# Optimization experiments

Measured on AMD Instinct MI355X. Metric: run time of the kernel, lower is better.

Reference implementation:

```python
import jax, jax.numpy as jnp
import numpy as np

N = 100000       # nodes
E = 1600000      # edges (avg degree 16)
F_IN = 128       # num_node_features
H = 128          # hidden_num
C = 40           # num_classes


def setup_inputs() -> dict:
    key = jax.random.key(0)
    k = jax.random.split(key, 6)
    x = jax.random.normal(k[0], (N, F_IN), dtype=jnp.float32)
    edge_index = jax.random.randint(k[1], (2, E), 0, N, dtype=jnp.int32)
    # Glorot-ish scaled params for the two GCNConv layers
    W1 = jax.random.normal(k[2], (F_IN, H), dtype=jnp.float32) * (1.0 / np.sqrt(F_IN))
    b1 = jnp.zeros((H,), dtype=jnp.float32)
    W2 = jax.random.normal(k[3], (H, C), dtype=jnp.float32) * (1.0 / np.sqrt(H))
    b2 = jnp.zeros((C,), dtype=jnp.float32)
    return {"x": x, "edge_index": edge_index, "W1": W1, "b1": b1, "W2": W2, "b2": b2}


def _gcn_conv(x, W, b, src, dst, n_nodes):
    """PyG GCNConv: add self-loops, symmetric normalization, linear transform.
    out[i] = sum_{j in N(i)} d_i^-1/2 d_j^-1/2 (x W)[j] + d_i^-1 (x W)[i] + b
    Self-loop contribution handled analytically (no edge concat).
    """
    h = x @ W                                            # [N, out]
    ones = jnp.ones((src.shape[0],), dtype=x.dtype)
    deg = jax.ops.segment_sum(ones, dst, num_segments=n_nodes) + 1.0  # +1 self-loop
    dinv = jax.lax.rsqrt(deg)                            # deg >= 1 always
    norm = dinv[src] * dinv[dst]                         # [E]
    msg = h[src] * norm[:, None]                         # [E, out] gather + scale
    agg = jax.ops.segment_sum(msg, dst, num_segments=n_nodes)
    agg = agg + h * (dinv * dinv)[:, None]               # self-loop term
    return agg + b


def reference(x, edge_index, W1, b1, W2, b2):
    # eval mode: F.dropout(training=False) is identity
    src, dst = edge_index[0], edge_index[1]
    h = jax.nn.relu(_gcn_conv(x, W1, b1, src, dst, N))
    out = _gcn_conv(h, W2, b2, src, dst, N)
    return out
```

## Files before the change

### kernel.cpp

```cpp
#include <hip/hip_runtime.h>
#include <hip/hip_fp16.h>


#define F_IN  128
#define F_H   128
#define F_OUT 40

#define BK_SHIFT 7
#define BK_MAX   1024
#define CHUNK    4096

typedef _Float16 half8v __attribute__((ext_vector_type(8)));
typedef float    f32x4  __attribute__((ext_vector_type(4)));


__global__ void k_prep(const float* __restrict__ W1, const float* __restrict__ W2,
                       __half* __restrict__ img1, __half* __restrict__ img2,
                       int* __restrict__ bcnt, int nbk) {
    int b = blockIdx.x;
    if (b < 64) {
        int idx = b * 256 + threadIdx.x;
        int j = idx >> 7, k = idx & 127;
        img1[j * 128 + (k ^ ((j & 7) << 3))] = __float2half_rn(W1[k * 128 + j]);
    } else if (b < 88) {
        int idx = (b - 64) * 256 + threadIdx.x;
        int j = idx >> 7, k = idx & 127;
        float v = (j < F_OUT) ? W2[k * F_OUT + j] : 0.f;
        img2[j * 128 + (k ^ ((j & 7) << 3))] = __float2half_rn(v);
    } else {
        for (int i = threadIdx.x; i < nbk; i += 256) bcnt[i] = 0;
    }
}


__global__ __launch_bounds__(256) void k_bscatter(const int* __restrict__ src,
                                                  const int* __restrict__ dst,
                                                  int* __restrict__ bcnt,
                                                  int* __restrict__ ebuf,
                                                  int e, int nbk, int cap) {
    __shared__ int hist[BK_MAX];
    __shared__ int base[BK_MAX];
    __shared__ int run[BK_MAX];
    int e0 = blockIdx.x * CHUNK;
    int e1 = min(e0 + CHUNK, e);
    for (int i = threadIdx.x; i < nbk; i += 256) { hist[i] = 0; run[i] = 0; }
    __syncthreads();
    for (int i = e0 + threadIdx.x; i < e1; i += 256)
        atomicAdd(&hist[dst[i] >> BK_SHIFT], 1);
    __syncthreads();
    for (int i = threadIdx.x; i < nbk; i += 256) {
        int c = hist[i];
        base[i] = c ? (cap * i + atomicAdd(&bcnt[i], c)) : 0;
    }
    __syncthreads();
    for (int i = e0 + threadIdx.x; i < e1; i += 256) {
        int d = dst[i];
        int b = d >> BK_SHIFT;
        int r = atomicAdd(&run[b], 1);
        ebuf[base[b] + r] = (src[i] << BK_SHIFT) | (d & ((1 << BK_SHIFT) - 1));
    }
}


__global__ __launch_bounds__(256) void k_bnode(const int* __restrict__ ebuf,
                                               const int* __restrict__ bcnt,
                                               int2* __restrict__ rbd,
                                               float* __restrict__ dinv,
                                               int* __restrict__ col,
                                               int n, int cap) {
    __shared__ int hist[128];
    __shared__ int sc[128];
    __shared__ int cur[128];
    const int b   = blockIdx.x;
    const int tid = threadIdx.x;
    const int e0 = b * cap;
    const int e1 = e0 + bcnt[b];

    if (tid < 128) hist[tid] = 0;
    __syncthreads();
    for (int i = e0 + tid; i < e1; i += 256)
        atomicAdd(&hist[ebuf[i] & 127], 1);
    __syncthreads();
    if (tid < 128) sc[tid] = hist[tid];
    __syncthreads();
    for (int off = 1; off < 128; off <<= 1) {
        int t = 0;
        if (tid < 128 && tid >= off) t = sc[tid - off];
        __syncthreads();
        if (tid < 128) sc[tid] += t;
        __syncthreads();
    }
    if (tid < 128) {
        int node = (b << BK_SHIFT) + tid;
        int excl = sc[tid] - hist[tid];
        if (node < n) {
            rbd[node] = make_int2(e0 + excl, hist[tid]);
            dinv[node] = rsqrtf((float)hist[tid] + 1.0f);
        }
        cur[tid] = e0 + excl;
    }
    __syncthreads();
    for (int i = e0 + tid; i < e1; i += 256) {
        int w = ebuf[i];
        int pos = atomicAdd(&cur[w & 127], 1);
        col[pos] = w >> BK_SHIFT;
    }
}


__global__ __launch_bounds__(256) void k_gemm1(const float* __restrict__ x,
                                               const __half* __restrict__ Wimg,
                                               const float* __restrict__ dinv,
                                               __half* __restrict__ h, int n) {
    __shared__ __half wlds[128 * 128];
    const int tid = threadIdx.x;
#pragma unroll
    for (int it = 0; it < 8; ++it) {
        int i = tid * 8 + it * 2048;
        *(uint4*)&wlds[i] = *(const uint4*)&Wimg[i];
    }

    const int l  = tid & 63;
    const int g  = l >> 4;
    const int r0 = blockIdx.x * 64 + (tid >> 6) * 16;
    int row = r0 + (l & 15);
    if (row > n - 1) row = n - 1;

    const float* xb = x + row * F_IN + g * 8;
    half8v afr[4];
#pragma unroll
    for (int kk = 0; kk < 4; ++kk) {
        float4 u0 = *(const float4*)(xb + kk * 32);
        float4 u1 = *(const float4*)(xb + kk * 32 + 4);
        half8v a;
        a[0] = (_Float16)u0.x; a[1] = (_Float16)u0.y;
        a[2] = (_Float16)u0.z; a[3] = (_Float16)u0.w;
        a[4] = (_Float16)u1.x; a[5] = (_Float16)u1.y;
        a[6] = (_Float16)u1.z; a[7] = (_Float16)u1.w;
        afr[kk] = a;
    }
    __syncthreads();

    const char* wb = (const char*)wlds;
    const int swz = (l & 7) << 4;
    f32x4 acc[8] = {};
#pragma unroll
    for (int ct = 0; ct < 8; ++ct) {
        const int base = (ct * 16 + (l & 15)) * 256;
#pragma unroll
        for (int kk = 0; kk < 4; ++kk) {
            half8v bfr = *(const half8v*)(wb + base + ((kk * 64 + g * 16) ^ swz));
            acc[ct] = __builtin_amdgcn_mfma_f32_16x16x32_f16(afr[kk], bfr, acc[ct], 0, 0, 0);
        }
    }

    const int orow0 = r0 + g * 4;
    float dv[4];
#pragma unroll
    for (int b = 0; b < 4; ++b) {
        int r = orow0 + b;
        dv[b] = (r < n) ? dinv[r] : 0.f;
    }
#pragma unroll
    for (int ct = 0; ct < 8; ++ct) {
#pragma unroll
        for (int b = 0; b < 4; ++b) {
            int r = orow0 + b;
            if (r < n)
                h[r * F_H + ct * 16 + (l & 15)] = __float2half_rn(acc[ct][b] * dv[b]);
        }
    }
}


#define UNPK8(A, u) { \
    float2 t0 = __half22float2(*(__half2*)&(u).x); \
    float2 t1 = __half22float2(*(__half2*)&(u).y); \
    float2 t2 = __half22float2(*(__half2*)&(u).z); \
    float2 t3 = __half22float2(*(__half2*)&(u).w); \
    A[0] += t0.x; A[1] += t0.y; A[2] += t1.x; A[3] += t1.y; \
    A[4] += t2.x; A[5] += t2.y; A[6] += t3.x; A[7] += t3.y; }

__global__ __launch_bounds__(256) void k_agg1r(const __half* __restrict__ h1s,
                                               const int2* __restrict__ rbd,
                                               const int* __restrict__ col,
                                               const float* __restrict__ dinv,
                                               const float* __restrict__ b1,
                                               __half* __restrict__ out1, int n) {
    int wid = (blockIdx.x * 256 + threadIdx.x) >> 6;
    int lane = threadIdx.x & 63;
    if (wid >= n) return;
    int2 bd = rbd[wid];
    int beg = bd.x, end = bd.x + bd.y;
    const int q = lane >> 4;
    const int f = lane & 15;
    const uint4* hb = (const uint4*)h1s + f;

    float ax[8] = {}, bx[8] = {};
    int idx = beg;
    for (; idx + 8 <= end; idx += 8) {
        int s0 = col[idx + q];
        int s1 = col[idx + 4 + q];
        uint4 u0 = hb[s0 << 4];
        uint4 u1 = hb[s1 << 4];
        UNPK8(ax, u0);
        UNPK8(bx, u1);
    }
    if (idx + 4 <= end) {
        int s = col[idx + q];
        uint4 u = hb[s << 4];
        UNPK8(ax, u);
        idx += 4;
    }
    int rem = end - idx;
    if (q < rem) {
        int s = col[idx + q];
        uint4 u = hb[s << 4];
        UNPK8(bx, u);
    }
#pragma unroll
    for (int j = 0; j < 8; ++j) ax[j] += bx[j];
#pragma unroll
    for (int j = 0; j < 8; ++j) {
        ax[j] += __shfl(ax[j], lane ^ 16);
        ax[j] += __shfl(ax[j], lane ^ 32);
    }
    if (q == 0) {
        uint4 hu = hb[wid << 4];
        float hv[8] = {};
        UNPK8(hv, hu);
        float di = dinv[wid];
        float4 bv0 = *(const float4*)&b1[8 * f];
        float4 bv1 = *(const float4*)&b1[8 * f + 4];
        float o[8];
        o[0] = fmaxf(fmaf(ax[0] + hv[0], di, bv0.x), 0.f);
        o[1] = fmaxf(fmaf(ax[1] + hv[1], di, bv0.y), 0.f);
        o[2] = fmaxf(fmaf(ax[2] + hv[2], di, bv0.z), 0.f);
        o[3] = fmaxf(fmaf(ax[3] + hv[3], di, bv0.w), 0.f);
        o[4] = fmaxf(fmaf(ax[4] + hv[4], di, bv1.x), 0.f);
        o[5] = fmaxf(fmaf(ax[5] + hv[5], di, bv1.y), 0.f);
        o[6] = fmaxf(fmaf(ax[6] + hv[6], di, bv1.z), 0.f);
        o[7] = fmaxf(fmaf(ax[7] + hv[7], di, bv1.w), 0.f);
        __half2 p0 = __floats2half2_rn(o[0], o[1]);
        __half2 p1 = __floats2half2_rn(o[2], o[3]);
        __half2 p2 = __floats2half2_rn(o[4], o[5]);
        __half2 p3 = __floats2half2_rn(o[6], o[7]);
        uint4 pk;
        pk.x = *(unsigned int*)&p0; pk.y = *(unsigned int*)&p1;
        pk.z = *(unsigned int*)&p2; pk.w = *(unsigned int*)&p3;
        *(uint4*)&out1[(wid << 7) + 8 * f] = pk;
    }
}


__global__ __launch_bounds__(256) void k_gemm2(const __half* __restrict__ xin,
                                               const __half* __restrict__ Wimg,
                                               const float* __restrict__ dinv,
                                               __half* __restrict__ h, int n) {
    __shared__ __half wlds[48 * 128];
    const int tid = threadIdx.x;
#pragma unroll
    for (int it = 0; it < 3; ++it) {
        int i = tid * 8 + it * 2048;
        *(uint4*)&wlds[i] = *(const uint4*)&Wimg[i];
    }

    const int l  = tid & 63;
    const int g  = l >> 4;
    const int r0 = blockIdx.x * 64 + (tid >> 6) * 16;
    int row = r0 + (l & 15);
    if (row > n - 1) row = n - 1;

    const __half* ab = xin + row * F_H + g * 8;
    half8v afr[4];
#pragma unroll
    for (int kk = 0; kk < 4; ++kk) afr[kk] = *(const half8v*)(ab + kk * 32);
    __syncthreads();

    const char* wb = (const char*)wlds;
    const int swz = (l & 7) << 4;
    f32x4 acc[3] = {};
#pragma unroll
    for (int ct = 0; ct < 3; ++ct) {
        const int base = (ct * 16 + (l & 15)) * 256;
#pragma unroll
        for (int kk = 0; kk < 4; ++kk) {
            half8v bfr = *(const half8v*)(wb + base + ((kk * 64 + g * 16) ^ swz));
            acc[ct] = __builtin_amdgcn_mfma_f32_16x16x32_f16(afr[kk], bfr, acc[ct], 0, 0, 0);
        }
    }

    const int orow0 = r0 + g * 4;
    float dv[4];
#pragma unroll
    for (int b = 0; b < 4; ++b) {
        int r = orow0 + b;
        dv[b] = (r < n) ? dinv[r] : 0.f;
    }
#pragma unroll
    for (int ct = 0; ct < 3; ++ct) {
        int c = ct * 16 + (l & 15);
#pragma unroll
        for (int b = 0; b < 4; ++b) {
            int r = orow0 + b;
            if (r < n && c < F_OUT)
                h[r * F_OUT + c] = __float2half_rn(acc[ct][b] * dv[b]);
        }
    }
}


#define UNPK4(A, u) { \
    float2 t0 = __half22float2(*(__half2*)&(u).x); \
    float2 t1 = __half22float2(*(__half2*)&(u).y); \
    A[0] += t0.x; A[1] += t0.y; A[2] += t1.x; A[3] += t1.y; }

__global__ __launch_bounds__(256) void k_agg2(const __half* __restrict__ h2s,
                                              const int2* __restrict__ rbd,
                                              const int* __restrict__ col,
                                              const float* __restrict__ dinv,
                                              const float* __restrict__ b2,
                                              float* __restrict__ out, int n) {
    int wid = (blockIdx.x * 256 + threadIdx.x) >> 6;
    int lane = threadIdx.x & 63;
    if (wid >= n) return;
    int g = lane / 10;
    int f = lane - g * 10;
    bool act = (g < 6);
    const uint2* hb = (const uint2*)h2s + f;
    int2 bd = rbd[wid];
    int beg = bd.x, end = bd.x + bd.y;

    float ax[4] = {}, bx[4] = {};
    int idx = beg;
    if (act) {
        for (; idx + 12 <= end; idx += 12) {
            int s0 = col[idx + g];
            int s1 = col[idx + 6 + g];
            uint2 u0 = hb[s0 * 10];
            uint2 u1 = hb[s1 * 10];
            UNPK4(ax, u0);
            UNPK4(bx, u1);
        }
        if (idx + 6 <= end) {
            int s = col[idx + g];
            uint2 u = hb[s * 10];
            UNPK4(ax, u);
            idx += 6;
        }
        int rem = end - idx;
        if (g < rem) {
            int s = col[idx + g];
            uint2 u = hb[s * 10];
            UNPK4(bx, u);
        }
    }
#pragma unroll
    for (int j = 0; j < 4; ++j) ax[j] += bx[j];
#pragma unroll
    for (int j = 0; j < 4; ++j) {
        float t = ax[j] + __shfl(ax[j], lane + 30);
        ax[j] = t + __shfl(t, lane + 10) + __shfl(t, lane + 20);
    }
    if (g == 0) {
        uint2 hu = hb[wid * 10];
        float hv[4] = {};
        UNPK4(hv, hu);
        float di = dinv[wid];
        float4 bv = *(const float4*)&b2[4 * f];
        float4 o;
        o.x = fmaf(ax[0] + hv[0], di, bv.x);
        o.y = fmaf(ax[1] + hv[1], di, bv.y);
        o.z = fmaf(ax[2] + hv[2], di, bv.z);
        o.w = fmaf(ax[3] + hv[3], di, bv.w);
        *(float4*)&out[wid * F_OUT + 4 * f] = o;
    }
}


extern "C" void kernel_launch(void* const* d_in, const int* in_sizes, int n_in,
                              void* d_out, int out_size, void* d_ws, size_t ws_size,
                              hipStream_t stream) {
    const float* x  = (const float*)d_in[0];
    const int*   ei = (const int*)d_in[1];
    const float* W1 = (const float*)d_in[2];
    const float* b1 = (const float*)d_in[3];
    const float* W2 = (const float*)d_in[4];
    const float* b2 = (const float*)d_in[5];
    float* out = (float*)d_out;

    const int N = in_sizes[0] / F_IN;
    const int E = in_sizes[1] / 2;
    const int* src = ei;
    const int* dst = ei + E;
    const int nbk = (N + (1 << BK_SHIFT) - 1) >> BK_SHIFT;
    const int cap = (((2 * E) / nbk) + 63) & ~63;

    char* ws = (char*)d_ws;
    size_t off = 0;
    auto alloc = [&](size_t bytes) -> void* {
        off = (off + 255) & ~(size_t)255;
        void* p = ws + off;
        off += bytes;
        return p;
    };
    float*  dinv    = (float*) alloc((size_t)N * 4);
    int2*   rbd     = (int2*)  alloc((size_t)N * 8);
    int*    bcnt    = (int*)   alloc(BK_MAX * 4);
    __half* W1img   = (__half*)alloc(128 * 128 * 2);
    __half* W2img   = (__half*)alloc(48 * 128 * 2);
    int*    ebuf    = (int*)   alloc((size_t)nbk * cap * 4);
    int*    col     = (int*)   alloc((size_t)nbk * cap * 4);
    __half* h1s     = (__half*)alloc((size_t)N * F_H * 2);
    __half* out1h   = (__half*)alloc((size_t)N * F_H * 2);
    __half* h2s     = h1s;

    const int gC = (E + CHUNK - 1) / CHUNK;

    k_prep    <<<89, 256, 0, stream>>>(W1, W2, W1img, W2img, bcnt, nbk);
    k_bscatter<<<gC, 256, 0, stream>>>(src, dst, bcnt, ebuf, E, nbk, cap);
    k_bnode   <<<nbk, 256, 0, stream>>>(ebuf, bcnt, rbd, dinv, col, N, cap);

    k_gemm1<<<(N + 63) / 64, 256, 0, stream>>>(x, W1img, dinv, h1s, N);
    k_agg1r<<<(N + 3) / 4, 256, 0, stream>>>(h1s, rbd, col, dinv, b1, out1h, N);
    k_gemm2<<<(N + 63) / 64, 256, 0, stream>>>(out1h, W2img, dinv, h2s, N);
    k_agg2 <<<(N + 3) / 4, 256, 0, stream>>>(h2s, rbd, col, dinv, b2, out, N);
}
```

Before: 185.2 us.

## Slice layer-1 features into 16-column blocks for cache-friendly aggregation

Stores the first GEMM output in a column-sliced layout: eight slices of 16 halves per node. Aggregation becomes a persistent-grid kernel where blockIdx selects a slice, so each slice's gathers work over a 3.2MB table that fits better in cache. The second GEMM reads its A operand from the same sliced layout. The cost is 8-byte gathers instead of 16-byte ones, each node's col list being read eight times, and more shuffle reductions.

```diff
diff --git a/kernel.cpp b/kernel.cpp
--- a/kernel.cpp
+++ b/kernel.cpp
@@ -167,88 +167,72 @@
         for (int b = 0; b < 4; ++b) {
             int r = orow0 + b;
             if (r < n)
-                h[r * F_H + ct * 16 + (l & 15)] = __float2half_rn(acc[ct][b] * dv[b]);
-        }
-    }
-}
-
-
-#define UNPK8(A, u) { \
-    float2 t0 = __half22float2(*(__half2*)&(u).x); \
-    float2 t1 = __half22float2(*(__half2*)&(u).y); \
-    float2 t2 = __half22float2(*(__half2*)&(u).z); \
-    float2 t3 = __half22float2(*(__half2*)&(u).w); \
-    A[0] += t0.x; A[1] += t0.y; A[2] += t1.x; A[3] += t1.y; \
-    A[4] += t2.x; A[5] += t2.y; A[6] += t3.x; A[7] += t3.y; }
-
-__global__ __launch_bounds__(256) void k_agg1r(const __half* __restrict__ h1s,
+                h[(size_t)ct * n * 16 + r * 16 + (l & 15)] =
+                    __float2half_rn(acc[ct][b] * dv[b]);
+        }
+    }
+}
+
+
+__global__ __launch_bounds__(256) void k_agg1s(const __half* __restrict__ hs,
                                                const int2* __restrict__ rbd,
                                                const int* __restrict__ col,
                                                const float* __restrict__ dinv,
                                                const float* __restrict__ b1,
-                                               __half* __restrict__ out1, int n) {
-    int wid = (blockIdx.x * 256 + threadIdx.x) >> 6;
-    int lane = threadIdx.x & 63;
-    if (wid >= n) return;
-    int2 bd = rbd[wid];
-    int beg = bd.x, end = bd.x + bd.y;
-    const int q = lane >> 4;
-    const int f = lane & 15;
-    const uint4* hb = (const uint4*)h1s + f;
-
-    float ax[8] = {}, bx[8] = {};
-    int idx = beg;
-    for (; idx + 8 <= end; idx += 8) {
-        int s0 = col[idx + q];
-        int s1 = col[idx + 4 + q];
-        uint4 u0 = hb[s0 << 4];
-        uint4 u1 = hb[s1 << 4];
-        UNPK8(ax, u0);
-        UNPK8(bx, u1);
-    }
-    if (idx + 4 <= end) {
-        int s = col[idx + q];
-        uint4 u = hb[s << 4];
-        UNPK8(ax, u);
-        idx += 4;
-    }
-    int rem = end - idx;
-    if (q < rem) {
-        int s = col[idx + q];
-        uint4 u = hb[s << 4];
-        UNPK8(bx, u);
-    }
-#pragma unroll
-    for (int j = 0; j < 8; ++j) ax[j] += bx[j];
-#pragma unroll
-    for (int j = 0; j < 8; ++j) {
-        ax[j] += __shfl(ax[j], lane ^ 16);
-        ax[j] += __shfl(ax[j], lane ^ 32);
-    }
-    if (q == 0) {
-        uint4 hu = hb[wid << 4];
-        float hv[8] = {};
-        UNPK8(hv, hu);
-        float di = dinv[wid];
-        float4 bv0 = *(const float4*)&b1[8 * f];
-        float4 bv1 = *(const float4*)&b1[8 * f + 4];
-        float o[8];
-        o[0] = fmaxf(fmaf(ax[0] + hv[0], di, bv0.x), 0.f);
-        o[1] = fmaxf(fmaf(ax[1] + hv[1], di, bv0.y), 0.f);
-        o[2] = fmaxf(fmaf(ax[2] + hv[2], di, bv0.z), 0.f);
-        o[3] = fmaxf(fmaf(ax[3] + hv[3], di, bv0.w), 0.f);
-        o[4] = fmaxf(fmaf(ax[4] + hv[4], di, bv1.x), 0.f);
-        o[5] = fmaxf(fmaf(ax[5] + hv[5], di, bv1.y), 0.f);
-        o[6] = fmaxf(fmaf(ax[6] + hv[6], di, bv1.z), 0.f);
-        o[7] = fmaxf(fmaf(ax[7] + hv[7], di, bv1.w), 0.f);
-        __half2 p0 = __floats2half2_rn(o[0], o[1]);
-        __half2 p1 = __floats2half2_rn(o[2], o[3]);
-        __half2 p2 = __floats2half2_rn(o[4], o[5]);
-        __half2 p3 = __floats2half2_rn(o[6], o[7]);
-        uint4 pk;
-        pk.x = *(unsigned int*)&p0; pk.y = *(unsigned int*)&p1;
-        pk.z = *(unsigned int*)&p2; pk.w = *(unsigned int*)&p3;
-        *(uint4*)&out1[(wid << 7) + 8 * f] = pk;
+                                               __half* __restrict__ outs,
+                                               int n, int nslcblk) {
+    const int slice = blockIdx.x & 7;
+    const int blk   = blockIdx.x >> 3;
+    const int wave  = threadIdx.x >> 6;
+    const int lane  = threadIdx.x & 63;
+    const int q = lane >> 2;
+    const int p = lane & 3;
+
+    const uint2* t = (const uint2*)hs + (size_t)slice * n * 4 + p;
+    __half* os = outs + (size_t)slice * n * 16;
+    const int wps = nslcblk * 4;
+
+    for (int node = blk * 4 + wave; node < n; node += wps) {
+        int2 bd = rbd[node];
+        int beg = bd.x, end = beg + bd.y;
+
+        float a0 = 0.f, a1 = 0.f, a2 = 0.f, a3 = 0.f;
+        for (int idx = beg; idx < end; idx += 16) {
+            int sl = idx + q;
+            if (sl < end) {
+                int s = col[sl];
+                uint2 u = t[s << 2];
+                float2 u0 = __half22float2(*(__half2*)&u.x);
+                float2 u1 = __half22float2(*(__half2*)&u.y);
+                a0 += u0.x; a1 += u0.y; a2 += u1.x; a3 += u1.y;
+            }
+        }
+        a0 += __shfl(a0, lane ^ 4);  a1 += __shfl(a1, lane ^ 4);
+        a2 += __shfl(a2, lane ^ 4);  a3 += __shfl(a3, lane ^ 4);
+        a0 += __shfl(a0, lane ^ 8);  a1 += __shfl(a1, lane ^ 8);
+        a2 += __shfl(a2, lane ^ 8);  a3 += __shfl(a3, lane ^ 8);
+        a0 += __shfl(a0, lane ^ 16); a1 += __shfl(a1, lane ^ 16);
+        a2 += __shfl(a2, lane ^ 16); a3 += __shfl(a3, lane ^ 16);
+        a0 += __shfl(a0, lane ^ 32); a1 += __shfl(a1, lane ^ 32);
+        a2 += __shfl(a2, lane ^ 32); a3 += __shfl(a3, lane ^ 32);
+
+        if (lane < 4) {
+            uint2 su = t[node << 2];
+            float2 s0 = __half22float2(*(__half2*)&su.x);
+            float2 s1 = __half22float2(*(__half2*)&su.y);
+            float di = dinv[node];
+            float4 bb = *(const float4*)&b1[slice * 16 + lane * 4];
+            float o0 = fmaxf(fmaf(a0 + s0.x, di, bb.x), 0.f);
+            float o1 = fmaxf(fmaf(a1 + s0.y, di, bb.y), 0.f);
+            float o2 = fmaxf(fmaf(a2 + s1.x, di, bb.z), 0.f);
+            float o3 = fmaxf(fmaf(a3 + s1.y, di, bb.w), 0.f);
+            __half2 h0 = __floats2half2_rn(o0, o1);
+            __half2 h1 = __floats2half2_rn(o2, o3);
+            uint2 pk;
+            pk.x = *(unsigned int*)&h0;
+            pk.y = *(unsigned int*)&h1;
+            *(uint2*)&os[node * 16 + lane * 4] = pk;
+        }
     }
 }
 
@@ -271,10 +255,13 @@
     int row = r0 + (l & 15);
     if (row > n - 1) row = n - 1;
 
-    const __half* ab = xin + row * F_H + g * 8;
     half8v afr[4];
 #pragma unroll
-    for (int kk = 0; kk < 4; ++kk) afr[kk] = *(const half8v*)(ab + kk * 32);
+    for (int kk = 0; kk < 4; ++kk) {
+        const __half* ab = xin + (size_t)(2 * kk + (g >> 1)) * n * 16
+                         + row * 16 + (g & 1) * 8;
+        afr[kk] = *(const half8v*)ab;
+    }
     __syncthreads();
 
     const char* wb = (const char*)wlds;
@@ -412,17 +399,18 @@
     int*    ebuf    = (int*)   alloc((size_t)nbk * cap * 4);
     int*    col     = (int*)   alloc((size_t)nbk * cap * 4);
     __half* h1s     = (__half*)alloc((size_t)N * F_H * 2);
-    __half* out1h   = (__half*)alloc((size_t)N * F_H * 2);
+    __half* out1s   = (__half*)alloc((size_t)N * F_H * 2);
     __half* h2s     = h1s;
 
     const int gC = (E + CHUNK - 1) / CHUNK;
+    const int nslcblk = 160;
 
     k_prep    <<<89, 256, 0, stream>>>(W1, W2, W1img, W2img, bcnt, nbk);
     k_bscatter<<<gC, 256, 0, stream>>>(src, dst, bcnt, ebuf, E, nbk, cap);
     k_bnode   <<<nbk, 256, 0, stream>>>(ebuf, bcnt, rbd, dinv, col, N, cap);
 
     k_gemm1<<<(N + 63) / 64, 256, 0, stream>>>(x, W1img, dinv, h1s, N);
-    k_agg1r<<<(N + 3) / 4, 256, 0, stream>>>(h1s, rbd, col, dinv, b1, out1h, N);
-    k_gemm2<<<(N + 63) / 64, 256, 0, stream>>>(out1h, W2img, dinv, h2s, N);
+    k_agg1s<<<8 * nslcblk, 256, 0, stream>>>(h1s, rbd, col, dinv, b1, out1s, N, nslcblk);
+    k_gemm2<<<(N + 63) / 64, 256, 0, stream>>>(out1s, W2img, dinv, h2s, N);
     k_agg2 <<<(N + 3) / 4, 256, 0, stream>>>(h2s, rbd, col, dinv, b2, out, N);
 }
```

New measurement: 369.4 us. 99.5% more time.
